# Kernel tuning notes

Hardware: AMD Instinct MI355X
Metric: run time of the kernel (lower is better)

## Reference

```python
import jax, jax.numpy as jnp
import numpy as np

BN_EPS = 1e-5
NEG_SLOPE = 0.2

def _bn(x, g, b, m, v):
    # inference-mode BatchNorm1d over the channel (last) axis
    return (x - m) * jax.lax.rsqrt(v + BN_EPS) * g + b

def _lrelu(x):
    return jnp.where(x >= 0, x, NEG_SLOPE * x)

def setup_inputs() -> dict:
    key = jax.random.key(0)
    ks = jax.random.split(key, 24)
    B, N, K, Cr, Cin, Cnb, Cout = 2, 65536, 16, 10, 64, 64, 128
    Ccat = Cin + Cnb
    return {
        'xyz': jax.random.normal(ks[0], (B, N, 3), jnp.float32),
        'feature': jax.random.normal(ks[1], (B, N, Cin), jnp.float32),
        'raw_neighbors_feature': jax.random.normal(ks[2], (B, N, K, Cr), jnp.float32),
        'neighbors_idx': jax.random.randint(ks[3], (B, N, K), 0, N, jnp.int32),
        'W_nb': jax.random.normal(ks[4], (Cr, Cnb), jnp.float32) * 0.3,
        'b_nb': jax.random.normal(ks[5], (Cnb,), jnp.float32),
        'g_nb': jax.random.uniform(ks[6], (Cnb,), jnp.float32),
        'be_nb': jax.random.normal(ks[7], (Cnb,), jnp.float32),
        'm_nb': jax.random.normal(ks[8], (Cnb,), jnp.float32),
        'v_nb': jax.random.uniform(ks[9], (Cnb,), jnp.float32),
        'W_attn': jax.random.normal(ks[10], (Ccat, Ccat), jnp.float32) * 0.09,
        'W_out': jax.random.normal(ks[11], (Ccat, Cout), jnp.float32) * 0.09,
        'b_out': jax.random.normal(ks[12], (Cout,), jnp.float32),
        'g_out': jax.random.uniform(ks[13], (Cout,), jnp.float32),
        'be_out': jax.random.normal(ks[14], (Cout,), jnp.float32),
        'm_out': jax.random.normal(ks[15], (Cout,), jnp.float32),
        'v_out': jax.random.uniform(ks[16], (Cout,), jnp.float32),
        'W_sc': jax.random.normal(ks[17], (Cin, Cout), jnp.float32) * 0.12,
        'b_sc': jax.random.normal(ks[18], (Cout,), jnp.float32),
        'g_sc': jax.random.uniform(ks[19], (Cout,), jnp.float32),
        'be_sc': jax.random.normal(ks[20], (Cout,), jnp.float32),
        'm_sc': jax.random.normal(ks[21], (Cout,), jnp.float32),
        'v_sc': jax.random.uniform(ks[22], (Cout,), jnp.float32),
    }

def reference(xyz, feature, raw_neighbors_feature, neighbors_idx,
              W_nb, b_nb, g_nb, be_nb, m_nb, v_nb,
              W_attn,
              W_out, b_out, g_out, be_out, m_out, v_out,
              W_sc, b_sc, g_sc, be_sc, m_sc, v_sc):
    # mlp_neighbor_fea: Linear -> BN1d -> leaky_relu(0.2) over raw neighbor features
    nb = _lrelu(_bn(jnp.einsum('bnkc,cd->bnkd', raw_neighbors_feature, W_nb) + b_nb,
                    g_nb, be_nb, m_nb, v_nb))              # [B,N,K,Cnb]
    # index_points: gather per-point neighbor features [B,N,K,Cin]
    gathered = jax.vmap(lambda f, i: f[i])(feature, neighbors_idx)
    fea = jnp.concatenate([gathered, nb], axis=-1)          # [B,N,K,Ccat]
    # attn pooling: softmax over neighbor axis K of a bias-free linear
    attn = jax.nn.softmax(jnp.einsum('bnkc,cd->bnkd', fea, W_attn), axis=2)
    pooled = jnp.sum(attn * fea, axis=2)                    # [B,N,Ccat]
    out_branch = _bn(pooled @ W_out + b_out, g_out, be_out, m_out, v_out)
    sc_branch = _bn(feature @ W_sc + b_sc, g_sc, be_sc, m_sc, v_sc)
    return _lrelu(sc_branch + out_branch)                   # [B,N,Cout]
```

## Files before the change

### kernel.cpp

```cpp
#include <hip/hip_runtime.h>


#define KNB   16
#define CR    10
#define CIN   64
#define CCAT  128
#define COUT  128
#define NPTS  131072
#define EPS   1e-5f
#define LOG2E 1.4426950408889634f

#define WS_WB   0
#define WS_W3   32768
#define WS_WNB  81920
#define WS_B3   86016
#define WS_BNB  86528
#define WS_FEA  87040

typedef const float* fp;
typedef short bf16x8 __attribute__((ext_vector_type(8)));
typedef float f32x4  __attribute__((ext_vector_type(4)));
typedef __bf16 bf16x2 __attribute__((ext_vector_type(2)));

__device__ __forceinline__ unsigned short f2bf(float x) {
    return __builtin_bit_cast(unsigned short, (__bf16)x);
}
__device__ __forceinline__ unsigned int pack2(float a, float b) {
    bf16x2 v; v.x = (__bf16)a; v.y = (__bf16)b;
    return __builtin_bit_cast(unsigned int, v);
}
__device__ __forceinline__ float bf2f(unsigned short h) {
    return __uint_as_float(((unsigned int)h) << 16);
}
__device__ __forceinline__ float lrelu(float x) { return fmaxf(x, 0.2f * x); }

__global__ __launch_bounds__(256) void lfa_prep(
    fp W_nb, fp b_nb, fp g_nb, fp be_nb, fp m_nb, fp v_nb,
    fp W_attn,
    fp W_out, fp b_out, fp g_out, fp be_out, fp m_out, fp v_out,
    fp W_sc,  fp b_sc,  fp g_sc,  fp be_sc,  fp m_sc,  fp v_sc,
    unsigned char* __restrict__ ws)
{
    const int t = blockIdx.x * 256 + threadIdx.x;
    if (t < 2048) {
        const int n0 = t >> 8, s = (t >> 6) & 3, ln = t & 63;
        const int n = (n0 << 4) + (ln & 15);
        unsigned int v[4];
        #pragma unroll
        for (int jj = 0; jj < 4; ++jj) {
            const int k = (s << 5) + ((ln >> 4) << 3) + jj * 2;
            v[jj] = pack2(W_attn[k * CCAT + n] * LOG2E,
                          W_attn[(k + 1) * CCAT + n] * LOG2E);
        }
        *(uint4*)(ws + WS_WB + t * 16) = make_uint4(v[0], v[1], v[2], v[3]);
    } else if (t < 5120) {
        const int e = t - 2048;
        const int t8 = e / 384, rem = e % 384, s = rem >> 6, ln = rem & 63;
        const int d = (t8 << 4) + (ln & 15);
        const float so = g_out[d] * rsqrtf(v_out[d] + EPS);
        const float ss = g_sc[d]  * rsqrtf(v_sc[d]  + EPS);
        unsigned int v[4];
        #pragma unroll
        for (int jj = 0; jj < 4; ++jj) {
            float a[2];
            #pragma unroll
            for (int h = 0; h < 2; ++h) {
                const int k = (s << 5) + ((ln >> 4) << 3) + jj * 2 + h;
                a[h] = (k < CCAT) ? W_out[k * COUT + d] * so
                                  : W_sc[(k - CCAT) * COUT + d] * ss;
            }
            v[jj] = pack2(a[0], a[1]);
        }
        *(uint4*)(ws + WS_W3 + e * 16) = make_uint4(v[0], v[1], v[2], v[3]);
    } else if (t < 5376) {
        const int e = t - 5120;
        const int n0 = e >> 6, ln = e & 63;
        const int n = (n0 << 4) + (ln & 15);
        const float sn = g_nb[n] * rsqrtf(v_nb[n] + EPS);
        unsigned int v[4];
        #pragma unroll
        for (int jj = 0; jj < 4; ++jj) {
            float a[2];
            #pragma unroll
            for (int h = 0; h < 2; ++h) {
                const int k = ((ln >> 4) << 3) + jj * 2 + h;
                a[h] = (k < CR) ? W_nb[k * 64 + n] * sn : 0.f;
            }
            v[jj] = pack2(a[0], a[1]);
        }
        *(uint4*)(ws + WS_WNB + e * 16) = make_uint4(v[0], v[1], v[2], v[3]);
    } else if (t < 5504) {
        const int d = t - 5376;
        const float so = g_out[d] * rsqrtf(v_out[d] + EPS);
        const float ss = g_sc[d]  * rsqrtf(v_sc[d]  + EPS);
        ((float*)(ws + WS_B3))[d] =
              (b_out[d] - m_out[d]) * so + be_out[d]
            + (b_sc[d]  - m_sc[d])  * ss + be_sc[d];
    } else if (t < 5568) {
        const int d = t - 5504;
        const float sn = g_nb[d] * rsqrtf(v_nb[d] + EPS);
        ((float*)(ws + WS_BNB))[d] = (b_nb[d] - m_nb[d]) * sn + be_nb[d];
    }
}

__global__ __launch_bounds__(256) void lfa_prep_fea(
    fp feature, unsigned char* __restrict__ ws)
{
    const int t = blockIdx.x * 256 + threadIdx.x;
    const size_t idx = (size_t)t * 8;
    if (idx < (size_t)NPTS * CIN) {
        const float4 f0 = *(const float4*)&feature[idx];
        const float4 f1 = *(const float4*)&feature[idx + 4];
        uint4 o;
        o.x = pack2(f0.x, f0.y); o.y = pack2(f0.z, f0.w);
        o.z = pack2(f1.x, f1.y); o.w = pack2(f1.z, f1.w);
        *(uint4*)(ws + WS_FEA + idx * 2) = o;
    }
}

__global__ __launch_bounds__(64, 2) void lfa_main_bf16(
    fp raw, const int* __restrict__ nidx,
    const unsigned char* __restrict__ ws, float* __restrict__ out)
{
    __shared__ __align__(16) unsigned short feaA[2][16][136];
    __shared__ __align__(16) unsigned short pooledA[16][200];

    const int lane = threadIdx.x;
    const int quad = lane >> 4;
    const int l15  = lane & 15;
    const int p0   = blockIdx.x * 16;
    const int b    = p0 >> 16;

    const unsigned short* feaT = (const unsigned short*)(ws + WS_FEA);
    const unsigned char*  wbp  = ws + WS_WB + ((size_t)lane << 4);

    float binb[4];
    #pragma unroll
    for (int j = 0; j < 4; ++j)
        binb[j] = ((const float*)(ws + WS_BNB))[j * 16 + l15];

    #pragma unroll 1
    for (int it = 0; it < 8; ++it) {
        const int pp0 = p0 + it * 2;

        int idxv = 0;
        if (lane < 32) idxv = nidx[pp0 * KNB + lane];

        if (lane < 32) {
            const int pt = lane >> 4, c4 = l15 * 4;
            const uint2 cf = *(const uint2*)&feaT[(size_t)(pp0 + pt) * CIN + c4];
            *(uint2*)&pooledA[it * 2 + pt][CCAT + c4] = cf;
        }

        uint2 gv[2][4];
        #pragma unroll
        for (int pt = 0; pt < 2; ++pt)
            #pragma unroll
            for (int i = 0; i < 4; ++i) {
                const int ni = __shfl(idxv, pt * 16 + i * 4 + quad, 64);
                gv[pt][i] = *(const uint2*)&feaT[(size_t)((b << 16) + ni) * CIN + l15 * 4];
            }

        bf16x8 anb[2];
        #pragma unroll
        for (int pt = 0; pt < 2; ++pt) {
            bf16x8 a = {0, 0, 0, 0, 0, 0, 0, 0};
            const float* rp = raw + (size_t)(pp0 + pt) * (KNB * CR) + l15 * CR;
            if (quad == 0) {
                const float2 r0 = *(const float2*)(rp + 0);
                const float2 r1 = *(const float2*)(rp + 2);
                const float2 r2 = *(const float2*)(rp + 4);
                const float2 r3 = *(const float2*)(rp + 6);
                a[0] = (short)f2bf(r0.x); a[1] = (short)f2bf(r0.y);
                a[2] = (short)f2bf(r1.x); a[3] = (short)f2bf(r1.y);
                a[4] = (short)f2bf(r2.x); a[5] = (short)f2bf(r2.y);
                a[6] = (short)f2bf(r3.x); a[7] = (short)f2bf(r3.y);
            } else if (quad == 1) {
                const float2 r4 = *(const float2*)(rp + 8);
                a[0] = (short)f2bf(r4.x); a[1] = (short)f2bf(r4.y);
            }
            anb[pt] = a;
        }

        float nbC[2][4][4];
        #pragma unroll
        for (int n0 = 0; n0 < 4; ++n0) {
            const bf16x8 bw = *(const bf16x8*)(ws + WS_WNB + ((n0 * 64 + lane) << 4));
            f32x4 c0 = {0.f, 0.f, 0.f, 0.f};
            f32x4 c1 = {0.f, 0.f, 0.f, 0.f};
            c0 = __builtin_amdgcn_mfma_f32_16x16x32_bf16(anb[0], bw, c0, 0, 0, 0);
            c1 = __builtin_amdgcn_mfma_f32_16x16x32_bf16(anb[1], bw, c1, 0, 0, 0);
            #pragma unroll
            for (int r = 0; r < 4; ++r) {
                const float x0 = lrelu(c0[r] + binb[n0]);
                const float x1 = lrelu(c1[r] + binb[n0]);
                nbC[0][n0][r] = x0;
                nbC[1][n0][r] = x1;
                feaA[0][quad * 4 + r][64 + n0 * 16 + l15] = f2bf(x0);
                feaA[1][quad * 4 + r][64 + n0 * 16 + l15] = f2bf(x1);
            }
        }

        #pragma unroll
        for (int pt = 0; pt < 2; ++pt)
            #pragma unroll
            for (int i = 0; i < 4; ++i)
                *(uint2*)&feaA[pt][i * 4 + quad][l15 * 4] = gv[pt][i];

        bf16x8 A[2][4];
        #pragma unroll
        for (int pt = 0; pt < 2; ++pt)
            #pragma unroll
            for (int s = 0; s < 4; ++s)
                A[pt][s] = *(const bf16x8*)&feaA[pt][l15][s * 32 + quad * 8];

        #pragma unroll
        for (int n0 = 0; n0 < 8; ++n0) {
            const bf16x8 wb0 = *(const bf16x8*)(wbp + (n0 * 4 + 0) * 1024);
            const bf16x8 wb1 = *(const bf16x8*)(wbp + (n0 * 4 + 1) * 1024);
            const bf16x8 wb2 = *(const bf16x8*)(wbp + (n0 * 4 + 2) * 1024);
            const bf16x8 wb3 = *(const bf16x8*)(wbp + (n0 * 4 + 3) * 1024);
            f32x4 c0 = {0.f, 0.f, 0.f, 0.f};
            f32x4 c1 = {0.f, 0.f, 0.f, 0.f};
            c0 = __builtin_amdgcn_mfma_f32_16x16x32_bf16(A[0][0], wb0, c0, 0, 0, 0);
            c1 = __builtin_amdgcn_mfma_f32_16x16x32_bf16(A[1][0], wb0, c1, 0, 0, 0);
            c0 = __builtin_amdgcn_mfma_f32_16x16x32_bf16(A[0][1], wb1, c0, 0, 0, 0);
            c1 = __builtin_amdgcn_mfma_f32_16x16x32_bf16(A[1][1], wb1, c1, 0, 0, 0);
            c0 = __builtin_amdgcn_mfma_f32_16x16x32_bf16(A[0][2], wb2, c0, 0, 0, 0);
            c1 = __builtin_amdgcn_mfma_f32_16x16x32_bf16(A[1][2], wb2, c1, 0, 0, 0);
            c0 = __builtin_amdgcn_mfma_f32_16x16x32_bf16(A[0][3], wb3, c0, 0, 0, 0);
            c1 = __builtin_amdgcn_mfma_f32_16x16x32_bf16(A[1][3], wb3, c1, 0, 0, 0);

            const float e00 = __builtin_amdgcn_exp2f(c0[0]);
            const float e01 = __builtin_amdgcn_exp2f(c0[1]);
            const float e02 = __builtin_amdgcn_exp2f(c0[2]);
            const float e03 = __builtin_amdgcn_exp2f(c0[3]);
            const float e10 = __builtin_amdgcn_exp2f(c1[0]);
            const float e11 = __builtin_amdgcn_exp2f(c1[1]);
            const float e12 = __builtin_amdgcn_exp2f(c1[2]);
            const float e13 = __builtin_amdgcn_exp2f(c1[3]);
            float den0 = e00 + e01 + e02 + e03;
            float den1 = e10 + e11 + e12 + e13;
            float num0, num1;
            if (n0 < 4) {
                num0 = e00 * bf2f(feaA[0][quad * 4 + 0][n0 * 16 + l15])
                     + e01 * bf2f(feaA[0][quad * 4 + 1][n0 * 16 + l15])
                     + e02 * bf2f(feaA[0][quad * 4 + 2][n0 * 16 + l15])
                     + e03 * bf2f(feaA[0][quad * 4 + 3][n0 * 16 + l15]);
                num1 = e10 * bf2f(feaA[1][quad * 4 + 0][n0 * 16 + l15])
                     + e11 * bf2f(feaA[1][quad * 4 + 1][n0 * 16 + l15])
                     + e12 * bf2f(feaA[1][quad * 4 + 2][n0 * 16 + l15])
                     + e13 * bf2f(feaA[1][quad * 4 + 3][n0 * 16 + l15]);
            } else {
                num0 = e00 * nbC[0][n0 - 4][0] + e01 * nbC[0][n0 - 4][1]
                     + e02 * nbC[0][n0 - 4][2] + e03 * nbC[0][n0 - 4][3];
                num1 = e10 * nbC[1][n0 - 4][0] + e11 * nbC[1][n0 - 4][1]
                     + e12 * nbC[1][n0 - 4][2] + e13 * nbC[1][n0 - 4][3];
            }
            num0 += __shfl_xor(num0, 16, 64);
            den0 += __shfl_xor(den0, 16, 64);
            num1 += __shfl_xor(num1, 16, 64);
            den1 += __shfl_xor(den1, 16, 64);
            num0 += __shfl_xor(num0, 32, 64);
            den0 += __shfl_xor(den0, 32, 64);
            num1 += __shfl_xor(num1, 32, 64);
            den1 += __shfl_xor(den1, 32, 64);
            const float pp0v = __fdividef(num0, den0);
            const float pp1v = __fdividef(num1, den1);
            if (quad == 0) {
                pooledA[it * 2 + 0][n0 * 16 + l15] = f2bf(pp0v);
                pooledA[it * 2 + 1][n0 * 16 + l15] = f2bf(pp1v);
            }
        }
    }

    bf16x8 A3[6];
    #pragma unroll
    for (int s = 0; s < 6; ++s)
        A3[s] = *(const bf16x8*)&pooledA[l15][s * 32 + quad * 8];
    #pragma unroll
    for (int t = 0; t < 8; ++t) {
        f32x4 c = {0.f, 0.f, 0.f, 0.f};
        #pragma unroll
        for (int s = 0; s < 6; ++s) {
            const bf16x8 bw = *(const bf16x8*)(ws + WS_W3 + (((t * 6 + s) * 64 + lane) << 4));
            c = __builtin_amdgcn_mfma_f32_16x16x32_bf16(A3[s], bw, c, 0, 0, 0);
        }
        const float bz = ((const float*)(ws + WS_B3))[t * 16 + l15];
        #pragma unroll
        for (int r = 0; r < 4; ++r)
            out[(size_t)(p0 + quad * 4 + r) * COUT + t * 16 + l15] = lrelu(c[r] + bz);
    }
}

__global__ __launch_bounds__(256, 2) void lfa_main_f32(
    fp feature, fp raw, const int* __restrict__ nidx,
    const unsigned char* __restrict__ ws, float* __restrict__ out)
{
    __shared__ __align__(16) unsigned short feaA[4][16][136];
    __shared__ __align__(16) unsigned short pooledA[4][16][200];

    const int tid  = threadIdx.x;
    const int w    = tid >> 6;
    const int lane = tid & 63;
    const int quad = lane >> 4;
    const int l15  = lane & 15;
    const int p0   = (blockIdx.x * 4 + w) * 16;
    const int b    = p0 >> 16;

    bf16x8 WB[8][4];
    #pragma unroll
    for (int n0 = 0; n0 < 8; ++n0)
        #pragma unroll
        for (int s = 0; s < 4; ++s)
            WB[n0][s] = *(const bf16x8*)(ws + WS_WB + (((n0 * 4 + s) * 64 + lane) << 4));

    float binb[4];
    #pragma unroll
    for (int j = 0; j < 4; ++j)
        binb[j] = ((const float*)(ws + WS_BNB))[j * 16 + l15];

    #pragma unroll 1
    for (int it = 0; it < 8; ++it) {
        const int pp0 = p0 + it * 2;

        int idxv = 0;
        if (lane < 32) idxv = nidx[pp0 * KNB + lane];

        if (lane < 32) {
            const int pt = lane >> 4, c4 = l15 * 4;
            const float4 cf = *(const float4*)&feature[(size_t)(pp0 + pt) * CIN + c4];
            uint2 pk; pk.x = pack2(cf.x, cf.y); pk.y = pack2(cf.z, cf.w);
            *(uint2*)&pooledA[w][it * 2 + pt][CCAT + c4] = pk;
        }

        #pragma unroll
        for (int pt = 0; pt < 2; ++pt) {
            const int p = pp0 + pt;

            float4 gv[4];
            #pragma unroll
            for (int i = 0; i < 4; ++i) {
                const int ni = __shfl(idxv, pt * 16 + i * 4 + quad, 64);
                gv[i] = *(const float4*)&feature[(size_t)((b << 16) + ni) * CIN + l15 * 4];
            }

            bf16x8 anb = {0, 0, 0, 0, 0, 0, 0, 0};
            {
                const float* rp = raw + (size_t)p * (KNB * CR) + l15 * CR;
                if (quad == 0) {
                    const float2 r0 = *(const float2*)(rp + 0);
                    const float2 r1 = *(const float2*)(rp + 2);
                    const float2 r2 = *(const float2*)(rp + 4);
                    const float2 r3 = *(const float2*)(rp + 6);
                    anb[0] = (short)f2bf(r0.x); anb[1] = (short)f2bf(r0.y);
                    anb[2] = (short)f2bf(r1.x); anb[3] = (short)f2bf(r1.y);
                    anb[4] = (short)f2bf(r2.x); anb[5] = (short)f2bf(r2.y);
                    anb[6] = (short)f2bf(r3.x); anb[7] = (short)f2bf(r3.y);
                } else if (quad == 1) {
                    const float2 r4 = *(const float2*)(rp + 8);
                    anb[0] = (short)f2bf(r4.x); anb[1] = (short)f2bf(r4.y);
                }
            }

            float nbC[4][4];
            #pragma unroll
            for (int n0 = 0; n0 < 4; ++n0) {
                const bf16x8 bw = *(const bf16x8*)(ws + WS_WNB + ((n0 * 64 + lane) << 4));
                f32x4 c = {0.f, 0.f, 0.f, 0.f};
                c = __builtin_amdgcn_mfma_f32_16x16x32_bf16(anb, bw, c, 0, 0, 0);
                #pragma unroll
                for (int r = 0; r < 4; ++r) {
                    const float x = lrelu(c[r] + binb[n0]);
                    nbC[n0][r] = x;
                    feaA[w][quad * 4 + r][64 + n0 * 16 + l15] = f2bf(x);
                }
            }

            #pragma unroll
            for (int i = 0; i < 4; ++i) {
                uint2 pk; pk.x = pack2(gv[i].x, gv[i].y); pk.y = pack2(gv[i].z, gv[i].w);
                *(uint2*)&feaA[w][i * 4 + quad][l15 * 4] = pk;
            }

            bf16x8 A[4];
            #pragma unroll
            for (int s = 0; s < 4; ++s)
                A[s] = *(const bf16x8*)&feaA[w][l15][s * 32 + quad * 8];

            #pragma unroll
            for (int n0 = 0; n0 < 8; ++n0) {
                f32x4 c = {0.f, 0.f, 0.f, 0.f};
                #pragma unroll
                for (int s = 0; s < 4; ++s)
                    c = __builtin_amdgcn_mfma_f32_16x16x32_bf16(A[s], WB[n0][s], c, 0, 0, 0);
                const float e0 = __builtin_amdgcn_exp2f(c[0]);
                const float e1 = __builtin_amdgcn_exp2f(c[1]);
                const float e2 = __builtin_amdgcn_exp2f(c[2]);
                const float e3 = __builtin_amdgcn_exp2f(c[3]);
                float den = e0 + e1 + e2 + e3;
                float num;
                if (n0 < 4) {
                    num = e0 * bf2f(feaA[w][quad * 4 + 0][n0 * 16 + l15])
                        + e1 * bf2f(feaA[w][quad * 4 + 1][n0 * 16 + l15])
                        + e2 * bf2f(feaA[w][quad * 4 + 2][n0 * 16 + l15])
                        + e3 * bf2f(feaA[w][quad * 4 + 3][n0 * 16 + l15]);
                } else {
                    num = e0 * nbC[n0 - 4][0] + e1 * nbC[n0 - 4][1]
                        + e2 * nbC[n0 - 4][2] + e3 * nbC[n0 - 4][3];
                }
                num += __shfl_xor(num, 16, 64);
                den += __shfl_xor(den, 16, 64);
                num += __shfl_xor(num, 32, 64);
                den += __shfl_xor(den, 32, 64);
                const float pp = __fdividef(num, den);
                if (quad == 0)
                    pooledA[w][it * 2 + pt][n0 * 16 + l15] = f2bf(pp);
            }
        }
    }

    bf16x8 A3[6];
    #pragma unroll
    for (int s = 0; s < 6; ++s)
        A3[s] = *(const bf16x8*)&pooledA[w][l15][s * 32 + quad * 8];
    #pragma unroll
    for (int t = 0; t < 8; ++t) {
        f32x4 c = {0.f, 0.f, 0.f, 0.f};
        #pragma unroll
        for (int s = 0; s < 6; ++s) {
            const bf16x8 bw = *(const bf16x8*)(ws + WS_W3 + (((t * 6 + s) * 64 + lane) << 4));
            c = __builtin_amdgcn_mfma_f32_16x16x32_bf16(A3[s], bw, c, 0, 0, 0);
        }
        const float bz = ((const float*)(ws + WS_B3))[t * 16 + l15];
        #pragma unroll
        for (int r = 0; r < 4; ++r)
            out[(size_t)(p0 + quad * 4 + r) * COUT + t * 16 + l15] = lrelu(c[r] + bz);
    }
}

extern "C" void kernel_launch(void* const* d_in, const int* in_sizes, int n_in,
                              void* d_out, int out_size, void* d_ws, size_t ws_size,
                              hipStream_t stream)
{
    fp feature = (fp)d_in[1];
    fp raw     = (fp)d_in[2];
    const int* nidx = (const int*)d_in[3];
    fp W_nb = (fp)d_in[4],  b_nb = (fp)d_in[5],  g_nb = (fp)d_in[6];
    fp be_nb = (fp)d_in[7], m_nb = (fp)d_in[8],  v_nb = (fp)d_in[9];
    fp W_attn = (fp)d_in[10];
    fp W_out = (fp)d_in[11], b_out = (fp)d_in[12], g_out = (fp)d_in[13];
    fp be_out = (fp)d_in[14], m_out = (fp)d_in[15], v_out = (fp)d_in[16];
    fp W_sc = (fp)d_in[17], b_sc = (fp)d_in[18], g_sc = (fp)d_in[19];
    fp be_sc = (fp)d_in[20], m_sc = (fp)d_in[21], v_sc = (fp)d_in[22];

    hipLaunchKernelGGL(lfa_prep, dim3(22), dim3(256), 0, stream,
                       W_nb, b_nb, g_nb, be_nb, m_nb, v_nb,
                       W_attn,
                       W_out, b_out, g_out, be_out, m_out, v_out,
                       W_sc, b_sc, g_sc, be_sc, m_sc, v_sc,
                       (unsigned char*)d_ws);

    const size_t need = (size_t)WS_FEA + (size_t)NPTS * CIN * 2;
    if (ws_size >= need) {
        hipLaunchKernelGGL(lfa_prep_fea, dim3(4096), dim3(256), 0, stream,
                           feature, (unsigned char*)d_ws);
        hipLaunchKernelGGL(lfa_main_bf16, dim3(8192), dim3(64), 0, stream,
                           raw, nidx, (const unsigned char*)d_ws, (float*)d_out);
    } else {
        hipLaunchKernelGGL(lfa_main_f32, dim3(2048), dim3(256), 0, stream,
                           feature, raw, nidx,
                           (const unsigned char*)d_ws, (float*)d_out);
    }
}
```

Baseline: 406.6 us.

## Software-pipeline neighbor gathers and raw feature loads across loop iterations

```diff
diff --git a/kernel.cpp b/kernel.cpp
--- a/kernel.cpp
+++ b/kernel.cpp
@@ -134,62 +134,94 @@
     const unsigned short* feaT = (const unsigned short*)(ws + WS_FEA);
     const unsigned char*  wbp  = ws + WS_WB + ((size_t)lane << 4);
 
+    #pragma unroll
+    for (int j = 0; j < 4; ++j) {
+        const int e   = j * 64 + lane;
+        const int row = e >> 4, c4 = (e & 15) * 4;
+        const uint2 cf = *(const uint2*)&feaT[(size_t)(p0 + row) * CIN + c4];
+        *(uint2*)&pooledA[row][CCAT + c4] = cf;
+    }
+
     float binb[4];
     #pragma unroll
     for (int j = 0; j < 4; ++j)
         binb[j] = ((const float*)(ws + WS_BNB))[j * 16 + l15];
 
+    bf16x8 WNBf[4];
+    #pragma unroll
+    for (int n0 = 0; n0 < 4; ++n0)
+        WNBf[n0] = *(const bf16x8*)(ws + WS_WNB + ((n0 * 64 + lane) << 4));
+
+    int idxv = 0;
+    if (lane < 32) idxv = nidx[p0 * KNB + lane];
+
+    float2 rw[2][4];
+    #pragma unroll
+    for (int pt = 0; pt < 2; ++pt) {
+        const float* rp = raw + (size_t)(p0 + pt) * (KNB * CR) + l15 * CR;
+        if (quad == 0) {
+            rw[pt][0] = *(const float2*)(rp + 0);
+            rw[pt][1] = *(const float2*)(rp + 2);
+            rw[pt][2] = *(const float2*)(rp + 4);
+            rw[pt][3] = *(const float2*)(rp + 6);
+        } else if (quad == 1) {
+            rw[pt][0] = *(const float2*)(rp + 8);
+        }
+    }
+
+    uint2 gv[2][4];
+    #pragma unroll
+    for (int pt = 0; pt < 2; ++pt)
+        #pragma unroll
+        for (int i = 0; i < 4; ++i) {
+            const int ni = __shfl(idxv, pt * 16 + i * 4 + quad, 64);
+            gv[pt][i] = *(const uint2*)&feaT[(size_t)((b << 16) + ni) * CIN + l15 * 4];
+        }
+
     #pragma unroll 1
     for (int it = 0; it < 8; ++it) {
-        const int pp0 = p0 + it * 2;
-
-        int idxv = 0;
-        if (lane < 32) idxv = nidx[pp0 * KNB + lane];
-
-        if (lane < 32) {
-            const int pt = lane >> 4, c4 = l15 * 4;
-            const uint2 cf = *(const uint2*)&feaT[(size_t)(pp0 + pt) * CIN + c4];
-            *(uint2*)&pooledA[it * 2 + pt][CCAT + c4] = cf;
-        }
-
-        uint2 gv[2][4];
-        #pragma unroll
-        for (int pt = 0; pt < 2; ++pt)
-            #pragma unroll
-            for (int i = 0; i < 4; ++i) {
-                const int ni = __shfl(idxv, pt * 16 + i * 4 + quad, 64);
-                gv[pt][i] = *(const uint2*)&feaT[(size_t)((b << 16) + ni) * CIN + l15 * 4];
-            }
+        const int  pp0  = p0 + it * 2;
+        const bool more = (it < 7);
 
         bf16x8 anb[2];
         #pragma unroll
         for (int pt = 0; pt < 2; ++pt) {
             bf16x8 a = {0, 0, 0, 0, 0, 0, 0, 0};
-            const float* rp = raw + (size_t)(pp0 + pt) * (KNB * CR) + l15 * CR;
             if (quad == 0) {
-                const float2 r0 = *(const float2*)(rp + 0);
-                const float2 r1 = *(const float2*)(rp + 2);
-                const float2 r2 = *(const float2*)(rp + 4);
-                const float2 r3 = *(const float2*)(rp + 6);
-                a[0] = (short)f2bf(r0.x); a[1] = (short)f2bf(r0.y);
-                a[2] = (short)f2bf(r1.x); a[3] = (short)f2bf(r1.y);
-                a[4] = (short)f2bf(r2.x); a[5] = (short)f2bf(r2.y);
-                a[6] = (short)f2bf(r3.x); a[7] = (short)f2bf(r3.y);
+                a[0] = (short)f2bf(rw[pt][0].x); a[1] = (short)f2bf(rw[pt][0].y);
+                a[2] = (short)f2bf(rw[pt][1].x); a[3] = (short)f2bf(rw[pt][1].y);
+                a[4] = (short)f2bf(rw[pt][2].x); a[5] = (short)f2bf(rw[pt][2].y);
+                a[6] = (short)f2bf(rw[pt][3].x); a[7] = (short)f2bf(rw[pt][3].y);
             } else if (quad == 1) {
-                const float2 r4 = *(const float2*)(rp + 8);
-                a[0] = (short)f2bf(r4.x); a[1] = (short)f2bf(r4.y);
+                a[0] = (short)f2bf(rw[pt][0].x); a[1] = (short)f2bf(rw[pt][0].y);
             }
             anb[pt] = a;
         }
 
+        int idxv_n = 0;
+        if (more && lane < 32) idxv_n = nidx[(pp0 + 2) * KNB + lane];
+        if (more) {
+            #pragma unroll
+            for (int pt = 0; pt < 2; ++pt) {
+                const float* rp = raw + (size_t)(pp0 + 2 + pt) * (KNB * CR) + l15 * CR;
+                if (quad == 0) {
+                    rw[pt][0] = *(const float2*)(rp + 0);
+                    rw[pt][1] = *(const float2*)(rp + 2);
+                    rw[pt][2] = *(const float2*)(rp + 4);
+                    rw[pt][3] = *(const float2*)(rp + 6);
+                } else if (quad == 1) {
+                    rw[pt][0] = *(const float2*)(rp + 8);
+                }
+            }
+        }
+
         float nbC[2][4][4];
         #pragma unroll
         for (int n0 = 0; n0 < 4; ++n0) {
-            const bf16x8 bw = *(const bf16x8*)(ws + WS_WNB + ((n0 * 64 + lane) << 4));
             f32x4 c0 = {0.f, 0.f, 0.f, 0.f};
             f32x4 c1 = {0.f, 0.f, 0.f, 0.f};
-            c0 = __builtin_amdgcn_mfma_f32_16x16x32_bf16(anb[0], bw, c0, 0, 0, 0);
-            c1 = __builtin_amdgcn_mfma_f32_16x16x32_bf16(anb[1], bw, c1, 0, 0, 0);
+            c0 = __builtin_amdgcn_mfma_f32_16x16x32_bf16(anb[0], WNBf[n0], c0, 0, 0, 0);
+            c1 = __builtin_amdgcn_mfma_f32_16x16x32_bf16(anb[1], WNBf[n0], c1, 0, 0, 0);
             #pragma unroll
             for (int r = 0; r < 4; ++r) {
                 const float x0 = lrelu(c0[r] + binb[n0]);
@@ -271,6 +303,23 @@
                 pooledA[it * 2 + 0][n0 * 16 + l15] = f2bf(pp0v);
                 pooledA[it * 2 + 1][n0 * 16 + l15] = f2bf(pp1v);
             }
+        }
+
+        if (more) {
+            uint2 gvn[2][4];
+            #pragma unroll
+            for (int pt = 0; pt < 2; ++pt)
+                #pragma unroll
+                for (int i = 0; i < 4; ++i) {
+                    const int ni = __shfl(idxv_n, pt * 16 + i * 4 + quad, 64);
+                    gvn[pt][i] = *(const uint2*)&feaT[(size_t)((b << 16) + ni) * CIN + l15 * 4];
+                }
+            #pragma unroll
+            for (int pt = 0; pt < 2; ++pt)
+                #pragma unroll
+                for (int i = 0; i < 4; ++i)
+                    gv[pt][i] = gvn[pt][i];
+            idxv = idxv_n;
         }
     }
 
```

After: 471.7 us. +16.0%, slower.

## Prefetch gathered neighbor features into swizzled LDS via async global_load_lds double buffer

Applied to the files above, without the earlier changes.

```diff
diff --git a/kernel.cpp b/kernel.cpp
--- a/kernel.cpp
+++ b/kernel.cpp
@@ -33,6 +33,17 @@
     return __uint_as_float(((unsigned int)h) << 16);
 }
 __device__ __forceinline__ float lrelu(float x) { return fmaxf(x, 0.2f * x); }
+
+__device__ __forceinline__ unsigned short* swzp(unsigned short (*h)[64], int row, int c) {
+    const int cg  = c >> 3;
+    const int off = row * 128 + (((cg ^ (row & 7)) << 4) | ((c & 7) << 1));
+    return (unsigned short*)((unsigned char*)h + off);
+}
+__device__ __forceinline__ const unsigned short* swzc(const unsigned short (*h)[64], int row, int c) {
+    const int cg  = c >> 3;
+    const int off = row * 128 + (((cg ^ (row & 7)) << 4) | ((c & 7) << 1));
+    return (const unsigned short*)((const unsigned char*)h + off);
+}
 
 __global__ __launch_bounds__(256) void lfa_prep(
     fp W_nb, fp b_nb, fp g_nb, fp be_nb, fp m_nb, fp v_nb,
@@ -122,7 +133,8 @@
     fp raw, const int* __restrict__ nidx,
     const unsigned char* __restrict__ ws, float* __restrict__ out)
 {
-    __shared__ __align__(16) unsigned short feaA[2][16][136];
+    __shared__ __align__(16) unsigned short feaG[2][2][16][64];
+    __shared__ __align__(16) unsigned short feaN[2][16][64];
     __shared__ __align__(16) unsigned short pooledA[16][200];
 
     const int lane = threadIdx.x;
@@ -134,32 +146,46 @@
     const unsigned short* feaT = (const unsigned short*)(ws + WS_FEA);
     const unsigned char*  wbp  = ws + WS_WB + ((size_t)lane << 4);
 
+    const int srcswz = ((lane & 7) ^ (lane >> 3)) << 4;
+    const int rowsh  = lane >> 3;
+
+    #pragma unroll
+    for (int j = 0; j < 4; ++j) {
+        const int e   = j * 64 + lane;
+        const int row = e >> 4, c4 = (e & 15) * 4;
+        const uint2 cf = *(const uint2*)&feaT[(size_t)(p0 + row) * CIN + c4];
+        *(uint2*)&pooledA[row][CCAT + c4] = cf;
+    }
+
     float binb[4];
     #pragma unroll
     for (int j = 0; j < 4; ++j)
         binb[j] = ((const float*)(ws + WS_BNB))[j * 16 + l15];
 
+    int idxv = 0;
+    if (lane < 32) idxv = nidx[p0 * KNB + lane];
+    #pragma unroll
+    for (int pt = 0; pt < 2; ++pt)
+        #pragma unroll
+        for (int i = 0; i < 2; ++i) {
+            const int ni = __shfl(idxv, pt * 16 + i * 8 + rowsh, 64);
+            const unsigned char* src = (const unsigned char*)feaT
+                + (((size_t)((b << 16) + ni)) << 7) + srcswz;
+            __builtin_amdgcn_global_load_lds(
+                (__attribute__((address_space(1))) const void*)src,
+                (__attribute__((address_space(3))) void*)
+                    ((unsigned char*)&feaG[0][pt][0][0] + i * 1024),
+                16, 0, 0);
+        }
+
+    int cur = 0;
     #pragma unroll 1
     for (int it = 0; it < 8; ++it) {
-        const int pp0 = p0 + it * 2;
-
-        int idxv = 0;
-        if (lane < 32) idxv = nidx[pp0 * KNB + lane];
-
-        if (lane < 32) {
-            const int pt = lane >> 4, c4 = l15 * 4;
-            const uint2 cf = *(const uint2*)&feaT[(size_t)(pp0 + pt) * CIN + c4];
-            *(uint2*)&pooledA[it * 2 + pt][CCAT + c4] = cf;
-        }
-
-        uint2 gv[2][4];
-        #pragma unroll
-        for (int pt = 0; pt < 2; ++pt)
-            #pragma unroll
-            for (int i = 0; i < 4; ++i) {
-                const int ni = __shfl(idxv, pt * 16 + i * 4 + quad, 64);
-                gv[pt][i] = *(const uint2*)&feaT[(size_t)((b << 16) + ni) * CIN + l15 * 4];
-            }
+        const int  pp0  = p0 + it * 2;
+        const bool more = (it < 7);
+
+        int idxn = 0;
+        if (more && lane < 32) idxn = nidx[(pp0 + 2) * KNB + lane];
 
         bf16x8 anb[2];
         #pragma unroll
@@ -196,23 +222,21 @@
                 const float x1 = lrelu(c1[r] + binb[n0]);
                 nbC[0][n0][r] = x0;
                 nbC[1][n0][r] = x1;
-                feaA[0][quad * 4 + r][64 + n0 * 16 + l15] = f2bf(x0);
-                feaA[1][quad * 4 + r][64 + n0 * 16 + l15] = f2bf(x1);
-            }
-        }
-
-        #pragma unroll
-        for (int pt = 0; pt < 2; ++pt)
-            #pragma unroll
-            for (int i = 0; i < 4; ++i)
-                *(uint2*)&feaA[pt][i * 4 + quad][l15 * 4] = gv[pt][i];
+                *swzp(feaN[0], quad * 4 + r, n0 * 16 + l15) = f2bf(x0);
+                *swzp(feaN[1], quad * 4 + r, n0 * 16 + l15) = f2bf(x1);
+            }
+        }
+
+        asm volatile("s_waitcnt vmcnt(0)" ::: "memory");
 
         bf16x8 A[2][4];
         #pragma unroll
-        for (int pt = 0; pt < 2; ++pt)
-            #pragma unroll
-            for (int s = 0; s < 4; ++s)
-                A[pt][s] = *(const bf16x8*)&feaA[pt][l15][s * 32 + quad * 8];
+        for (int pt = 0; pt < 2; ++pt) {
+            A[pt][0] = *(const bf16x8*)swzc(feaG[cur][pt], l15, 0  + quad * 8);
+            A[pt][1] = *(const bf16x8*)swzc(feaG[cur][pt], l15, 32 + quad * 8);
+            A[pt][2] = *(const bf16x8*)swzc(feaN[pt],      l15, 0  + quad * 8);
+            A[pt][3] = *(const bf16x8*)swzc(feaN[pt],      l15, 32 + quad * 8);
+        }
 
         #pragma unroll
         for (int n0 = 0; n0 < 8; ++n0) {
@@ -231,6 +255,22 @@
             c0 = __builtin_amdgcn_mfma_f32_16x16x32_bf16(A[0][3], wb3, c0, 0, 0, 0);
             c1 = __builtin_amdgcn_mfma_f32_16x16x32_bf16(A[1][3], wb3, c1, 0, 0, 0);
 
+            if (n0 == 3 && more) {
+                #pragma unroll
+                for (int pt = 0; pt < 2; ++pt)
+                    #pragma unroll
+                    for (int i = 0; i < 2; ++i) {
+                        const int ni = __shfl(idxn, pt * 16 + i * 8 + rowsh, 64);
+                        const unsigned char* src = (const unsigned char*)feaT
+                            + (((size_t)((b << 16) + ni)) << 7) + srcswz;
+                        __builtin_amdgcn_global_load_lds(
+                            (__attribute__((address_space(1))) const void*)src,
+                            (__attribute__((address_space(3))) void*)
+                                ((unsigned char*)&feaG[cur ^ 1][pt][0][0] + i * 1024),
+                            16, 0, 0);
+                    }
+            }
+
             const float e00 = __builtin_amdgcn_exp2f(c0[0]);
             const float e01 = __builtin_amdgcn_exp2f(c0[1]);
             const float e02 = __builtin_amdgcn_exp2f(c0[2]);
@@ -243,14 +283,14 @@
             float den1 = e10 + e11 + e12 + e13;
             float num0, num1;
             if (n0 < 4) {
-                num0 = e00 * bf2f(feaA[0][quad * 4 + 0][n0 * 16 + l15])
-                     + e01 * bf2f(feaA[0][quad * 4 + 1][n0 * 16 + l15])
-                     + e02 * bf2f(feaA[0][quad * 4 + 2][n0 * 16 + l15])
-                     + e03 * bf2f(feaA[0][quad * 4 + 3][n0 * 16 + l15]);
-                num1 = e10 * bf2f(feaA[1][quad * 4 + 0][n0 * 16 + l15])
-                     + e11 * bf2f(feaA[1][quad * 4 + 1][n0 * 16 + l15])
-                     + e12 * bf2f(feaA[1][quad * 4 + 2][n0 * 16 + l15])
-                     + e13 * bf2f(feaA[1][quad * 4 + 3][n0 * 16 + l15]);
+                num0 = e00 * bf2f(*swzc(feaG[cur][0], quad * 4 + 0, n0 * 16 + l15))
+                     + e01 * bf2f(*swzc(feaG[cur][0], quad * 4 + 1, n0 * 16 + l15))
+                     + e02 * bf2f(*swzc(feaG[cur][0], quad * 4 + 2, n0 * 16 + l15))
+                     + e03 * bf2f(*swzc(feaG[cur][0], quad * 4 + 3, n0 * 16 + l15));
+                num1 = e10 * bf2f(*swzc(feaG[cur][1], quad * 4 + 0, n0 * 16 + l15))
+                     + e11 * bf2f(*swzc(feaG[cur][1], quad * 4 + 1, n0 * 16 + l15))
+                     + e12 * bf2f(*swzc(feaG[cur][1], quad * 4 + 2, n0 * 16 + l15))
+                     + e13 * bf2f(*swzc(feaG[cur][1], quad * 4 + 3, n0 * 16 + l15));
             } else {
                 num0 = e00 * nbC[0][n0 - 4][0] + e01 * nbC[0][n0 - 4][1]
                      + e02 * nbC[0][n0 - 4][2] + e03 * nbC[0][n0 - 4][3];
@@ -272,6 +312,8 @@
                 pooledA[it * 2 + 1][n0 * 16 + l15] = f2bf(pp1v);
             }
         }
+
+        cur ^= 1;
     }
 
     bf16x8 A3[6];
```

New measurement: 457.3 us. 1.12x slower.
